# Optimization experiments

Measured on AMD Instinct MI355X. Metric: run time of the kernel, lower is better.

## Reference

```python
import jax, jax.numpy as jnp
import numpy as np

V, E, H, OUT, L = 32000, 512, 512, 2, 2
S, B = 512, 64


def setup_inputs() -> dict:
    key = jax.random.key(0)
    ks = jax.random.split(key, 8)
    sc_w = float(np.sqrt(6.0 / (H + (E + H))))  # xavier_uniform bound-ish scale
    inp = {
        "texts": jax.random.randint(ks[0], (S, B), 0, V, dtype=jnp.int64),
        "emb": jax.random.normal(ks[1], (V, E), jnp.float32) * 0.05,
        "Wf": jax.random.normal(ks[2], (L, H, E + H), jnp.float32) * sc_w,
        "bf": jnp.zeros((L, H, 1), jnp.float32),
        "Wi": jax.random.normal(ks[3], (L, H, E + H), jnp.float32) * sc_w,
        "bi": jnp.zeros((L, H, 1), jnp.float32),
        "Wo": jax.random.normal(ks[4], (L, H, E + H), jnp.float32) * sc_w,
        "bo": jnp.zeros((L, H, 1), jnp.float32),
        "Wc": jax.random.normal(ks[5], (L, H, E + H), jnp.float32) * sc_w,
        "bc": jnp.zeros((L, H, 1), jnp.float32),
        "Wy": jax.random.normal(ks[6], (OUT, H), jnp.float32) * 0.05,
        "by": jnp.zeros((OUT, 1), jnp.float32),
    }
    return inp


def reference(texts, emb, Wf, bf, Wi, bi, Wo, bo, Wc, bc, Wy, by):
    seq_len, batch = texts.shape
    num_layers, hidden = Wf.shape[0], Wf.shape[1]
    # embedded: [S, E, B] (matches torch permute(1,2,0) of [B,S,E])
    x_seq = jnp.transpose(emb[texts], (0, 2, 1))

    h0 = jnp.zeros((hidden, batch), x_seq.dtype)
    c0 = jnp.zeros((hidden, batch), x_seq.dtype)

    def step(carry, x):
        h, c = carry  # NOTE: single (h, c) shared across layers, as in source
        for l in range(num_layers):
            cat = jnp.concatenate([h, x], axis=0)  # [H+E, B]
            ft = jax.nn.sigmoid(Wf[l] @ cat + bf[l])
            it = jax.nn.sigmoid(Wi[l] @ cat + bi[l])
            chat = jnp.tanh(Wc[l] @ cat + bc[l])
            c = ft * c + it * chat
            ot = jax.nn.sigmoid(Wo[l] @ cat + bo[l])
            h = ot * jnp.tanh(c)
            x = h
        return (h, c), None

    (h, _), _ = jax.lax.scan(step, (h0, c0), x_seq)
    y = h.T @ Wy.T + by.T  # [B, OUT]
    return jnp.squeeze(y, axis=1) if y.shape[1] == 1 else y
```

## Files before the change

kernel.cpp:

```cpp
#include <hip/hip_runtime.h>


typedef _Float16 f16;
typedef _Float16 f16x8 __attribute__((ext_vector_type(8)));
typedef float f32x4 __attribute__((ext_vector_type(4)));
typedef unsigned int u32;
typedef unsigned long long u64;
typedef unsigned short u16;

constexpr int Hn = 512, En = 512, Bn = 64, Sn = 512, OUTn = 2;
constexpr int NG = 4, GB = 32, BS = 16, RPB = 16;
constexpr int NB = NG * GB;
constexpr int NT = 512;
constexpr int RING = 16;
constexpr u32 SENT = 0xFFFFFFFFu;

constexpr size_t XB_OFF = 0;
constexpr size_t XB_SZ  = (size_t)NG * Sn * 16 * 64 * 16;
constexpr size_t RG_OFF = XB_OFF + XB_SZ;
constexpr size_t RG_SZ  = (size_t)NG * RING * 16384;

__device__ __forceinline__ float sig_(float x) { return 1.f / (1.f + expf(-x)); }

__device__ __forceinline__ void astore(u32* p, u32 v) {
  __hip_atomic_store(p, v, __ATOMIC_RELAXED, __HIP_MEMORY_SCOPE_AGENT);
}
__device__ __forceinline__ u64 aload64(const u64* p) {
  return __hip_atomic_load(p, __ATOMIC_RELAXED, __HIP_MEMORY_SCOPE_AGENT);
}
__device__ __forceinline__ bool okw(u64 x) {
  return ((u32)x != SENT) && ((u32)(x >> 32) != SENT);
}
__device__ __forceinline__ void poll2(const u64* p0, const u64* p1, f16x8& a, f16x8& b) {
  union U { f16x8 v; u64 q[2]; } ua, ub;
  int guard = 0;
  for (;;) {
    ua.q[0] = aload64(p0); ua.q[1] = aload64(p0 + 1);
    ub.q[0] = aload64(p1); ub.q[1] = aload64(p1 + 1);
    if (okw(ua.q[0]) && okw(ua.q[1]) && okw(ub.q[0]) && okw(ub.q[1])) break;
    if (++guard > (1 << 21)) break;
  }
  a = ua.v; b = ub.v;
}

union uf16 { f16 f; u16 u; };

__device__ __forceinline__ int fl_idx(int k, int col) {
  return (((k >> 5) * 64 + (((k >> 3) & 3) * 16) + col) << 3) + (k & 7);
}

__global__ void __launch_bounds__(256) xb_fill(
    const int* __restrict__ texts, const float* __restrict__ emb,
    f16x8* __restrict__ xb)
{
  const int bidx = blockIdx.x;
  const int g = bidx >> 9, t = bidx & (Sn - 1);
  const int tid = threadIdx.x;
  f16x8* dst = xb + (size_t)bidx * 1024;
  for (int slot = tid; slot < 1024; slot += 256) {
    int s = slot >> 6, sl = slot & 63, kg = sl >> 4, b = sl & 15;
    int idx = texts[t * Bn + g * BS + b];
    const float* er = emb + (size_t)idx * En + s * 32 + kg * 8;
    f16x8 v;
    #pragma unroll
    for (int j = 0; j < 8; ++j) v[j] = (f16)er[j];
    dst[slot] = v;
  }
}

__global__ void __launch_bounds__(NT) lstm_mfma(
    const float* __restrict__ Wf, const float* __restrict__ bf,
    const float* __restrict__ Wi, const float* __restrict__ bi,
    const float* __restrict__ Wo, const float* __restrict__ bo,
    const float* __restrict__ Wc, const float* __restrict__ bc,
    const float* __restrict__ Wy, const float* __restrict__ by,
    float* __restrict__ out, const f16x8* __restrict__ xb,
    u32* __restrict__ ringBase)
{
  __shared__ f16x8 sWAh[4][16][64];
  __shared__ f16x8 sXB[16][64];
  __shared__ f16x8 sHB[1024];
  __shared__ float sAccP[2][64][17];
  __shared__ float sAccX[64][17];
  __shared__ float sBiasX[64], sBias1[64];
  __shared__ float sC[16][16];
  __shared__ float sRed[16][2][4];

  const int tid = threadIdx.x;
  const int bid = blockIdx.x;
  const int g = bid & 3;
  const int rank = bid >> 2;
  const int w = tid >> 6, l = tid & 63;
  const int mt = w & 3, kh = w >> 2;
  const int col = l & 15, rb = (l >> 4) << 2;

  const float* Wg[4] = {Wf, Wi, Wc, Wo};
  const float* Bg[4] = {bf, bi, bc, bo};

  u32* ringG = ringBase + (size_t)g * RING * 4096;
  const f16x8* xbG = xb + (size_t)g * Sn * 1024;

  for (int i = 0; i < 8; ++i) {
    int slot = tid * 8 + i;
    int sl = slot & 63, s = (slot >> 6) & 15, m4 = slot >> 10;
    const float* row = Wg[m4] + (size_t)(rank * RPB + (sl & 15)) * (En + Hn);
    int k0 = s * 32 + (sl >> 4) * 8;
    f16x8 v;
    #pragma unroll
    for (int j = 0; j < 8; ++j) v[j] = (f16)row[k0 + j];
    sWAh[m4][s][sl] = v;
  }
  f16x8 afr1[8];
  {
    const float* row = Wg[mt] + (size_t)(Hn + rank * RPB + (l & 15)) * (En + Hn);
    #pragma unroll
    for (int i = 0; i < 8; ++i) {
      int k0 = (kh * 8 + i) * 32 + (l >> 4) * 8;
      f16x8 v;
      #pragma unroll
      for (int j = 0; j < 8; ++j) v[j] = (f16)(row[k0 + j] + row[k0 + j + Hn]);
      afr1[i] = v;
    }
  }
  f16x8 axf[16];
  if (kh == 1) {
    const float* row = Wg[mt] + (size_t)(rank * RPB + (l & 15)) * (En + Hn);
    #pragma unroll
    for (int i = 0; i < 16; ++i) {
      int k0 = Hn + i * 32 + (l >> 4) * 8;
      f16x8 v;
      #pragma unroll
      for (int j = 0; j < 8; ++j) v[j] = (f16)row[k0 + j];
      axf[i] = v;
    }
  }
  if (tid < 64) {
    int gate = tid >> 4, hr = tid & 15;
    sBiasX[tid] = Bg[gate][rank * RPB + hr];
    sBias1[tid] = Bg[gate][Hn + rank * RPB + hr];
  }
  if (tid < 256) sC[tid >> 4][tid & 15] = 0.f;
  if (w >= 4) {
    #pragma unroll
    for (int j = 0; j < 4; ++j) sXB[(w - 4) * 4 + j][l] = xbG[((w - 4) * 4 + j) * 64 + l];
  }
  __syncthreads();
  if (kh == 1) {
    f32x4 acc = {0.f, 0.f, 0.f, 0.f};
    #pragma unroll
    for (int s = 0; s < 16; ++s)
      acc = __builtin_amdgcn_mfma_f32_16x16x32_f16(axf[s], sXB[s][l], acc, 0, 0, 0);
    #pragma unroll
    for (int v = 0; v < 4; ++v) sAccX[mt * 16 + rb + v][col] = acc[v];
  }

  for (int t = 0; t < Sn; ++t) {
    const int qA = 2 * t;
    u32* bufRA = ringG + (size_t)(qA & 15) * 4096;
    u32* bufWA = ringG + (size_t)((qA + 1) & 15) * 4096;
    u32* bufCA = ringG + (size_t)((qA + 9) & 15) * 4096;

    if (tid >= 128 && tid < 256) astore(bufCA + rank * 128 + (tid - 128), SENT);
    f16x8 xp[4];
    if (w >= 4) {
      const int tn = (t + 1 < Sn) ? t + 1 : t;
      const f16x8* xbt = xbG + (size_t)tn * 1024;
      #pragma unroll
      for (int j = 0; j < 4; ++j) xp[j] = xbt[((w - 4) * 4 + j) * 64 + l];
    }
    {
      const u64* src = (const u64*)bufRA;
      f16x8 a, b;
      poll2(src + (w * 128 + l) * 2, src + (w * 128 + 64 + l) * 2, a, b);
      sHB[w * 128 + l] = a; sHB[w * 128 + 64 + l] = b;
    }
    if (w >= 4) {
      #pragma unroll
      for (int j = 0; j < 4; ++j) sXB[(w - 4) * 4 + j][l] = xp[j];
    }
    __syncthreads();
    {
      f32x4 acc = {0.f, 0.f, 0.f, 0.f};
      #pragma unroll
      for (int i = 0; i < 8; ++i) {
        int s = kh * 8 + i;
        acc = __builtin_amdgcn_mfma_f32_16x16x32_f16(sWAh[mt][s][l], sHB[s * 64 + l], acc, 0, 0, 0);
      }
      #pragma unroll
      for (int v = 0; v < 4; ++v) sAccP[kh][mt * 16 + rb + v][col] = acc[v];
    }
    __syncthreads();
    if (tid < 128) {
      int q8 = tid >> 4, b = tid & 15;
      u32 pk = 0;
      #pragma unroll
      for (int j = 0; j < 2; ++j) {
        int hr = 2 * q8 + j;
        float af = sAccP[0][ 0 + hr][b] + sAccP[1][ 0 + hr][b] + sAccX[ 0 + hr][b] + sBiasX[ 0 + hr];
        float ai = sAccP[0][16 + hr][b] + sAccP[1][16 + hr][b] + sAccX[16 + hr][b] + sBiasX[16 + hr];
        float ac = sAccP[0][32 + hr][b] + sAccP[1][32 + hr][b] + sAccX[32 + hr][b] + sBiasX[32 + hr];
        float ao = sAccP[0][48 + hr][b] + sAccP[1][48 + hr][b] + sAccX[48 + hr][b] + sBiasX[48 + hr];
        float ft = sig_(af), it = sig_(ai), ch = tanhf(ac), ot = sig_(ao);
        float c = ft * sC[hr][b] + it * ch;
        sC[hr][b] = c;
        uf16 hv; hv.f = (f16)(ot * tanhf(c));
        pk |= (u32)hv.u << (16 * j);
      }
      int k0 = rank * RPB + 2 * q8;
      int slot = (k0 >> 5) * 64 + ((k0 >> 3) & 3) * 16 + b;
      astore(bufWA + slot * 4 + (q8 & 3), pk);
    }

    u32* bufWB = ringG + (size_t)((qA + 2) & 15) * 4096;
    u32* bufCB = ringG + (size_t)((qA + 10) & 15) * 4096;
    if (tid >= 128 && tid < 256) astore(bufCB + rank * 128 + (tid - 128), SENT);
    {
      const u64* src = (const u64*)bufWA;
      f16x8 a, b;
      poll2(src + (w * 128 + l) * 2, src + (w * 128 + 64 + l) * 2, a, b);
      sHB[w * 128 + l] = a; sHB[w * 128 + 64 + l] = b;
    }
    __syncthreads();
    {
      f32x4 acc = {0.f, 0.f, 0.f, 0.f};
      #pragma unroll
      for (int i = 0; i < 8; ++i)
        acc = __builtin_amdgcn_mfma_f32_16x16x32_f16(afr1[i], sHB[(kh * 8 + i) * 64 + l], acc, 0, 0, 0);
      #pragma unroll
      for (int v = 0; v < 4; ++v) sAccP[kh][mt * 16 + rb + v][col] = acc[v];
    }
    __syncthreads();
    if (tid < 128) {
      int q8 = tid >> 4, b = tid & 15;
      u32 pk = 0;
      #pragma unroll
      for (int j = 0; j < 2; ++j) {
        int hr = 2 * q8 + j;
        float af = sAccP[0][ 0 + hr][b] + sAccP[1][ 0 + hr][b] + sBias1[ 0 + hr];
        float ai = sAccP[0][16 + hr][b] + sAccP[1][16 + hr][b] + sBias1[16 + hr];
        float ac = sAccP[0][32 + hr][b] + sAccP[1][32 + hr][b] + sBias1[32 + hr];
        float ao = sAccP[0][48 + hr][b] + sAccP[1][48 + hr][b] + sBias1[48 + hr];
        float ft = sig_(af), it = sig_(ai), ch = tanhf(ac), ot = sig_(ao);
        float c = ft * sC[hr][b] + it * ch;
        sC[hr][b] = c;
        uf16 hv; hv.f = (f16)(ot * tanhf(c));
        pk |= (u32)hv.u << (16 * j);
      }
      int k0 = rank * RPB + 2 * q8;
      int slot = (k0 >> 5) * 64 + ((k0 >> 3) & 3) * 16 + b;
      astore(bufWB + slot * 4 + (q8 & 3), pk);
    }
    if (kh == 1 && t + 1 < Sn) {
      f32x4 acc = {0.f, 0.f, 0.f, 0.f};
      #pragma unroll
      for (int s = 0; s < 16; ++s)
        acc = __builtin_amdgcn_mfma_f32_16x16x32_f16(axf[s], sXB[s][l], acc, 0, 0, 0);
      #pragma unroll
      for (int v = 0; v < 4; ++v) sAccX[mt * 16 + rb + v][col] = acc[v];
    }
  }

  if (rank == 0) {
    const u64* fin = (const u64*)(ringG + (size_t)((2 * Sn) & 15) * 4096);
    u64* dst = (u64*)sHB;
    for (int i = tid; i < 2048; i += NT) {
      u64 v = aload64(fin + i);
      int guard = 0;
      while (!okw(v)) { v = aload64(fin + i); if (++guard > (1 << 21)) break; }
      dst[i] = v;
    }
    __syncthreads();
    const f16* tmp = (const f16*)sHB;
    if (tid < 128) {
      int b = tid >> 3, o = (tid >> 2) & 1, kc = tid & 3;
      float p = 0.f;
      for (int kk = 0; kk < 128; ++kk) {
        int k = kc * 128 + kk;
        p += (float)tmp[fl_idx(k, b)] * Wy[o * Hn + k];
      }
      sRed[b][o][kc] = p;
    }
    __syncthreads();
    if (tid < 32) {
      int b2 = tid >> 1, o2 = tid & 1;
      float s = by[o2];
      #pragma unroll
      for (int q = 0; q < 4; ++q) s += sRed[b2][o2][q];
      out[(g * BS + b2) * OUTn + o2] = s;
    }
  }
}

extern "C" void kernel_launch(void* const* d_in, const int* in_sizes, int n_in,
                              void* d_out, int out_size, void* d_ws, size_t ws_size,
                              hipStream_t stream) {
  const int*   texts = (const int*)d_in[0];
  const float* emb   = (const float*)d_in[1];
  const float* Wf    = (const float*)d_in[2];
  const float* bf    = (const float*)d_in[3];
  const float* Wi    = (const float*)d_in[4];
  const float* bi    = (const float*)d_in[5];
  const float* Wo    = (const float*)d_in[6];
  const float* bo    = (const float*)d_in[7];
  const float* Wc    = (const float*)d_in[8];
  const float* bc    = (const float*)d_in[9];
  const float* Wy    = (const float*)d_in[10];
  const float* by    = (const float*)d_in[11];
  float* out = (float*)d_out;

  f16x8* xbuf    = (f16x8*)((char*)d_ws + XB_OFF);
  u32*   ringBase = (u32*)((char*)d_ws + RG_OFF);

  hipMemsetAsync((void*)ringBase, 0xFF, RG_SZ, stream);
  for (int g = 0; g < NG; ++g)
    hipMemsetAsync((void*)((char*)ringBase + (size_t)g * RING * 16384), 0x00, 16384, stream);

  xb_fill<<<dim3(NG * Sn), dim3(256), 0, stream>>>(texts, emb, xbuf);

  void* args[] = {(void*)&Wf, (void*)&bf, (void*)&Wi, (void*)&bi,
                  (void*)&Wo, (void*)&bo, (void*)&Wc, (void*)&bc, (void*)&Wy, (void*)&by,
                  (void*)&out, (void*)&xbuf, (void*)&ringBase};
  hipLaunchCooperativeKernel((const void*)lstm_mfma, dim3(NB), dim3(NT), args, 0, stream);
}
```

Baseline: 2.669 ms.

## Pack two batch groups per block with per-half LDS flag sync

Halves the grid from 128 to 64 blocks, so each block serves two batch groups, with each 4-wave half handling one group. Block-wide __syncthreads inside the time loop are replaced by LDS flag spinning between the waves of a half. Global ring polling now uses one 16-byte load with the sc1 cache bit per fragment. The input projection is computed directly from global memory by all waves after each step, and each wave does two MFMA gate tiles. The aim is fewer blocks taking part in the cross-block handoff and less barrier stall, at the cost of more work per block and fragile hand-rolled intra-block synchronisation.

Result: slower. 4.717 ms (+76.7%).

```diff
diff --git a/kernel.cpp b/kernel.cpp
--- a/kernel.cpp
+++ b/kernel.cpp
@@ -9,9 +9,8 @@
 typedef unsigned short u16;
 
 constexpr int Hn = 512, En = 512, Bn = 64, Sn = 512, OUTn = 2;
-constexpr int NG = 4, GB = 32, BS = 16, RPB = 16;
-constexpr int NB = NG * GB;
-constexpr int NT = 512;
+constexpr int NG = 4, BS = 16, RPB = 16;
+constexpr int NB = 64, NT = 512;
 constexpr int RING = 16;
 constexpr u32 SENT = 0xFFFFFFFFu;
 
@@ -31,16 +30,34 @@
 __device__ __forceinline__ bool okw(u64 x) {
   return ((u32)x != SENT) && ((u32)(x >> 32) != SENT);
 }
-__device__ __forceinline__ void poll2(const u64* p0, const u64* p1, f16x8& a, f16x8& b) {
-  union U { f16x8 v; u64 q[2]; } ua, ub;
+
+__device__ __forceinline__ f16x8 poll16(const u32* p) {
+  union { f16x8 v; u32 d[4]; } u;
   int guard = 0;
-  for (;;) {
-    ua.q[0] = aload64(p0); ua.q[1] = aload64(p0 + 1);
-    ub.q[0] = aload64(p1); ub.q[1] = aload64(p1 + 1);
-    if (okw(ua.q[0]) && okw(ua.q[1]) && okw(ub.q[0]) && okw(ub.q[1])) break;
-    if (++guard > (1 << 21)) break;
-  }
-  a = ua.v; b = ub.v;
+  do {
+    asm volatile("global_load_dwordx4 %0, %1, off sc1\n\ts_waitcnt vmcnt(0)"
+                 : "=&v"(u.v) : "v"(p) : "memory");
+    if ((u.d[0] != SENT) & (u.d[1] != SENT) & (u.d[2] != SENT) & (u.d[3] != SENT)) break;
+  } while (++guard < (1 << 17));
+  return u.v;
+}
+
+__device__ __forceinline__ void spin_ge(volatile u32* f, u32 q) {
+  int guard = 0;
+  while (*f < q) { if (++guard > (1 << 17)) break; }
+  __builtin_amdgcn_sched_barrier(0);
+}
+__device__ __forceinline__ void spin4(volatile u32* f, u32 q) {
+  int guard = 0;
+  while (f[0] < q || f[1] < q || f[2] < q || f[3] < q) {
+    if (++guard > (1 << 17)) break;
+  }
+  __builtin_amdgcn_sched_barrier(0);
+}
+__device__ __forceinline__ void set_flag(volatile u32* f, u32 q, int lane) {
+  asm volatile("s_waitcnt lgkmcnt(0)" ::: "memory");
+  __builtin_amdgcn_sched_barrier(0);
+  if (lane == 0) *f = q;
 }
 
 union uf16 { f16 f; u16 u; };
@@ -78,20 +95,25 @@
     u32* __restrict__ ringBase)
 {
   __shared__ f16x8 sWAh[4][16][64];
-  __shared__ f16x8 sXB[16][64];
-  __shared__ f16x8 sHB[1024];
-  __shared__ float sAccP[2][64][17];
-  __shared__ float sAccX[64][17];
+  __shared__ f16x8 sHB[2][1024];
+  __shared__ float sAccP[2][2][64][17];
+  __shared__ float sAccX[2][64][17];
   __shared__ float sBiasX[64], sBias1[64];
-  __shared__ float sC[16][16];
-  __shared__ float sRed[16][2][4];
+  __shared__ float sC[2][16][16];
+  __shared__ float sRed[2][16][2][4];
+  __shared__ volatile u32 sStg[2][4];
+  __shared__ volatile u32 sAcF[2][4];
+  __shared__ volatile u32 sGtF[2][2];
 
   const int tid = threadIdx.x;
   const int bid = blockIdx.x;
-  const int g = bid & 3;
-  const int rank = bid >> 2;
+  const int rank = bid >> 1;
+  const int jj = bid & 1;
   const int w = tid >> 6, l = tid & 63;
-  const int mt = w & 3, kh = w >> 2;
+  const int s = w >> 2;
+  const int u = w & 3;
+  const int p = u & 1, kh = u >> 1;
+  const int g = jj * 2 + s;
   const int col = l & 15, rb = (l >> 4) << 2;
 
   const float* Wg[4] = {Wf, Wi, Wc, Wo};
@@ -102,29 +124,30 @@
 
   for (int i = 0; i < 8; ++i) {
     int slot = tid * 8 + i;
-    int sl = slot & 63, s = (slot >> 6) & 15, m4 = slot >> 10;
+    int sl = slot & 63, ss = (slot >> 6) & 15, m4 = slot >> 10;
     const float* row = Wg[m4] + (size_t)(rank * RPB + (sl & 15)) * (En + Hn);
-    int k0 = s * 32 + (sl >> 4) * 8;
+    int k0 = ss * 32 + (sl >> 4) * 8;
     f16x8 v;
     #pragma unroll
     for (int j = 0; j < 8; ++j) v[j] = (f16)row[k0 + j];
-    sWAh[m4][s][sl] = v;
-  }
-  f16x8 afr1[8];
-  {
-    const float* row = Wg[mt] + (size_t)(Hn + rank * RPB + (l & 15)) * (En + Hn);
+    sWAh[m4][ss][sl] = v;
+  }
+  f16x8 afr1[2][8];
+  #pragma unroll
+  for (int mi = 0; mi < 2; ++mi) {
+    const float* row = Wg[2 * p + mi] + (size_t)(Hn + rank * RPB + (l & 15)) * (En + Hn);
     #pragma unroll
     for (int i = 0; i < 8; ++i) {
       int k0 = (kh * 8 + i) * 32 + (l >> 4) * 8;
       f16x8 v;
       #pragma unroll
       for (int j = 0; j < 8; ++j) v[j] = (f16)(row[k0 + j] + row[k0 + j + Hn]);
-      afr1[i] = v;
+      afr1[mi][i] = v;
     }
   }
   f16x8 axf[16];
-  if (kh == 1) {
-    const float* row = Wg[mt] + (size_t)(rank * RPB + (l & 15)) * (En + Hn);
+  {
+    const float* row = Wg[u] + (size_t)(rank * RPB + (l & 15)) * (En + Hn);
     #pragma unroll
     for (int i = 0; i < 16; ++i) {
       int k0 = Hn + i * 32 + (l >> 4) * 8;
@@ -139,155 +162,182 @@
     sBiasX[tid] = Bg[gate][rank * RPB + hr];
     sBias1[tid] = Bg[gate][Hn + rank * RPB + hr];
   }
-  if (tid < 256) sC[tid >> 4][tid & 15] = 0.f;
-  if (w >= 4) {
-    #pragma unroll
-    for (int j = 0; j < 4; ++j) sXB[(w - 4) * 4 + j][l] = xbG[((w - 4) * 4 + j) * 64 + l];
-  }
+  if (tid < 512) sC[tid >> 8][(tid >> 4) & 15][tid & 15] = 0.f;
+  if (tid < 4) { sStg[0][tid] = 0; sStg[1][tid] = 0; sAcF[0][tid] = 0; sAcF[1][tid] = 0; }
+  if (tid < 2) { sGtF[0][tid] = 0; sGtF[1][tid] = 0; }
   __syncthreads();
-  if (kh == 1) {
-    f32x4 acc = {0.f, 0.f, 0.f, 0.f};
-    #pragma unroll
-    for (int s = 0; s < 16; ++s)
-      acc = __builtin_amdgcn_mfma_f32_16x16x32_f16(axf[s], sXB[s][l], acc, 0, 0, 0);
-    #pragma unroll
-    for (int v = 0; v < 4; ++v) sAccX[mt * 16 + rb + v][col] = acc[v];
-  }
+
+  {
+    f32x4 ax = {0.f, 0.f, 0.f, 0.f};
+    #pragma unroll
+    for (int ks = 0; ks < 16; ++ks)
+      ax = __builtin_amdgcn_mfma_f32_16x16x32_f16(axf[ks], xbG[ks * 64 + l], ax, 0, 0, 0);
+    #pragma unroll
+    for (int v = 0; v < 4; ++v) sAccX[s][u * 16 + rb + v][col] = ax[v];
+  }
+
+  const int fbase = kh * 512 + p * 256;
 
   for (int t = 0; t < Sn; ++t) {
-    const int qA = 2 * t;
-    u32* bufRA = ringG + (size_t)(qA & 15) * 4096;
-    u32* bufWA = ringG + (size_t)((qA + 1) & 15) * 4096;
-    u32* bufCA = ringG + (size_t)((qA + 9) & 15) * 4096;
-
-    if (tid >= 128 && tid < 256) astore(bufCA + rank * 128 + (tid - 128), SENT);
-    f16x8 xp[4];
-    if (w >= 4) {
-      const int tn = (t + 1 < Sn) ? t + 1 : t;
-      const f16x8* xbt = xbG + (size_t)tn * 1024;
-      #pragma unroll
-      for (int j = 0; j < 4; ++j) xp[j] = xbt[((w - 4) * 4 + j) * 64 + l];
-    }
+    u32* rdA = ringG + (size_t)((2 * t) & 15) * 4096;
+    u32* wrA = ringG + (size_t)((2 * t + 1) & 15) * 4096;
+    u32* clA = ringG + (size_t)((2 * t + 9) & 15) * 4096;
+
     {
-      const u64* src = (const u64*)bufRA;
-      f16x8 a, b;
-      poll2(src + (w * 128 + l) * 2, src + (w * 128 + 64 + l) * 2, a, b);
-      sHB[w * 128 + l] = a; sHB[w * 128 + 64 + l] = b;
-    }
-    if (w >= 4) {
-      #pragma unroll
-      for (int j = 0; j < 4; ++j) sXB[(w - 4) * 4 + j][l] = xp[j];
-    }
-    __syncthreads();
+      const u32 q = 2 * t + 1;
+      f16x8 fr0 = poll16(rdA + (fbase + 0 * 64 + l) * 4);
+      f16x8 fr1 = poll16(rdA + (fbase + 1 * 64 + l) * 4);
+      f16x8 fr2 = poll16(rdA + (fbase + 2 * 64 + l) * 4);
+      f16x8 fr3 = poll16(rdA + (fbase + 3 * 64 + l) * 4);
+      spin4(&sAcF[s][0], q - 1);
+      sHB[s][fbase + 0 * 64 + l] = fr0;
+      sHB[s][fbase + 1 * 64 + l] = fr1;
+      sHB[s][fbase + 2 * 64 + l] = fr2;
+      sHB[s][fbase + 3 * 64 + l] = fr3;
+      set_flag(&sStg[s][u], q, l);
+      spin_ge(&sStg[s][u ^ 1], q);
+      spin_ge(&sGtF[s][0], q - 1);
+      spin_ge(&sGtF[s][1], q - 1);
+      f32x4 a0 = {0.f, 0.f, 0.f, 0.f}, a1 = {0.f, 0.f, 0.f, 0.f};
+      #pragma unroll
+      for (int i = 0; i < 8; ++i) {
+        int ks = kh * 8 + i;
+        f16x8 bf = sHB[s][ks * 64 + l];
+        a0 = __builtin_amdgcn_mfma_f32_16x16x32_f16(sWAh[2 * p + 0][ks][l], bf, a0, 0, 0, 0);
+        a1 = __builtin_amdgcn_mfma_f32_16x16x32_f16(sWAh[2 * p + 1][ks][l], bf, a1, 0, 0, 0);
+      }
+      #pragma unroll
+      for (int v = 0; v < 4; ++v) {
+        sAccP[s][kh][(2 * p + 0) * 16 + rb + v][col] = a0[v];
+        sAccP[s][kh][(2 * p + 1) * 16 + rb + v][col] = a1[v];
+      }
+      set_flag(&sAcF[s][u], q, l);
+      if (u < 2) {
+        spin4(&sAcF[s][0], q);
+        int gt = u * 64 + l, q8 = gt >> 4, b = gt & 15;
+        u32 pk = 0;
+        #pragma unroll
+        for (int j = 0; j < 2; ++j) {
+          int hr = 2 * q8 + j;
+          float af = sAccP[s][0][ 0 + hr][b] + sAccP[s][1][ 0 + hr][b] + sAccX[s][ 0 + hr][b] + sBiasX[ 0 + hr];
+          float ai = sAccP[s][0][16 + hr][b] + sAccP[s][1][16 + hr][b] + sAccX[s][16 + hr][b] + sBiasX[16 + hr];
+          float ac = sAccP[s][0][32 + hr][b] + sAccP[s][1][32 + hr][b] + sAccX[s][32 + hr][b] + sBiasX[32 + hr];
+          float ao = sAccP[s][0][48 + hr][b] + sAccP[s][1][48 + hr][b] + sAccX[s][48 + hr][b] + sBiasX[48 + hr];
+          float ft = sig_(af), it = sig_(ai), ch = tanhf(ac), ot = sig_(ao);
+          float c = ft * sC[s][hr][b] + it * ch;
+          sC[s][hr][b] = c;
+          uf16 hv; hv.f = (f16)(ot * tanhf(c));
+          pk |= (u32)hv.u << (16 * j);
+        }
+        int k0 = rank * RPB + 2 * q8;
+        int slot = (k0 >> 5) * 64 + ((k0 >> 3) & 3) * 16 + b;
+        astore(wrA + slot * 4 + (q8 & 3), pk);
+        __builtin_amdgcn_sched_barrier(0);
+        if (l == 0) sGtF[s][u] = q;
+      } else {
+        astore(clA + rank * 128 + (u - 2) * 64 + l, SENT);
+      }
+    }
+
     {
-      f32x4 acc = {0.f, 0.f, 0.f, 0.f};
+      const u32 q = 2 * t + 2;
+      u32* rdB = wrA;
+      u32* wrB = ringG + (size_t)((2 * t + 2) & 15) * 4096;
+      u32* clB = ringG + (size_t)((2 * t + 10) & 15) * 4096;
+      f16x8 fr0 = poll16(rdB + (fbase + 0 * 64 + l) * 4);
+      f16x8 fr1 = poll16(rdB + (fbase + 1 * 64 + l) * 4);
+      f16x8 fr2 = poll16(rdB + (fbase + 2 * 64 + l) * 4);
+      f16x8 fr3 = poll16(rdB + (fbase + 3 * 64 + l) * 4);
+      spin4(&sAcF[s][0], q - 1);
+      sHB[s][fbase + 0 * 64 + l] = fr0;
+      sHB[s][fbase + 1 * 64 + l] = fr1;
+      sHB[s][fbase + 2 * 64 + l] = fr2;
+      sHB[s][fbase + 3 * 64 + l] = fr3;
+      set_flag(&sStg[s][u], q, l);
+      spin_ge(&sStg[s][u ^ 1], q);
+      spin_ge(&sGtF[s][0], q - 1);
+      spin_ge(&sGtF[s][1], q - 1);
+      f32x4 a0 = {0.f, 0.f, 0.f, 0.f}, a1 = {0.f, 0.f, 0.f, 0.f};
       #pragma unroll
       for (int i = 0; i < 8; ++i) {
-        int s = kh * 8 + i;
-        acc = __builtin_amdgcn_mfma_f32_16x16x32_f16(sWAh[mt][s][l], sHB[s * 64 + l], acc, 0, 0, 0);
-      }
-      #pragma unroll
-      for (int v = 0; v < 4; ++v) sAccP[kh][mt * 16 + rb + v][col] = acc[v];
-    }
-    __syncthreads();
-    if (tid < 128) {
-      int q8 = tid >> 4, b = tid & 15;
-      u32 pk = 0;
-      #pragma unroll
-      for (int j = 0; j < 2; ++j) {
-        int hr = 2 * q8 + j;
-        float af = sAccP[0][ 0 + hr][b] + sAccP[1][ 0 + hr][b] + sAccX[ 0 + hr][b] + sBiasX[ 0 + hr];
-        float ai = sAccP[0][16 + hr][b] + sAccP[1][16 + hr][b] + sAccX[16 + hr][b] + sBiasX[16 + hr];
-        float ac = sAccP[0][32 + hr][b] + sAccP[1][32 + hr][b] + sAccX[32 + hr][b] + sBiasX[32 + hr];
-        float ao = sAccP[0][48 + hr][b] + sAccP[1][48 + hr][b] + sAccX[48 + hr][b] + sBiasX[48 + hr];
-        float ft = sig_(af), it = sig_(ai), ch = tanhf(ac), ot = sig_(ao);
-        float c = ft * sC[hr][b] + it * ch;
-        sC[hr][b] = c;
-        uf16 hv; hv.f = (f16)(ot * tanhf(c));
-        pk |= (u32)hv.u << (16 * j);
-      }
-      int k0 = rank * RPB + 2 * q8;
-      int slot = (k0 >> 5) * 64 + ((k0 >> 3) & 3) * 16 + b;
-      astore(bufWA + slot * 4 + (q8 & 3), pk);
-    }
-
-    u32* bufWB = ringG + (size_t)((qA + 2) & 15) * 4096;
-    u32* bufCB = ringG + (size_t)((qA + 10) & 15) * 4096;
-    if (tid >= 128 && tid < 256) astore(bufCB + rank * 128 + (tid - 128), SENT);
-    {
-      const u64* src = (const u64*)bufWA;
-      f16x8 a, b;
-      poll2(src + (w * 128 + l) * 2, src + (w * 128 + 64 + l) * 2, a, b);
-      sHB[w * 128 + l] = a; sHB[w * 128 + 64 + l] = b;
-    }
-    __syncthreads();
-    {
-      f32x4 acc = {0.f, 0.f, 0.f, 0.f};
-      #pragma unroll
-      for (int i = 0; i < 8; ++i)
-        acc = __builtin_amdgcn_mfma_f32_16x16x32_f16(afr1[i], sHB[(kh * 8 + i) * 64 + l], acc, 0, 0, 0);
-      #pragma unroll
-      for (int v = 0; v < 4; ++v) sAccP[kh][mt * 16 + rb + v][col] = acc[v];
-    }
-    __syncthreads();
-    if (tid < 128) {
-      int q8 = tid >> 4, b = tid & 15;
-      u32 pk = 0;
-      #pragma unroll
-      for (int j = 0; j < 2; ++j) {
-        int hr = 2 * q8 + j;
-        float af = sAccP[0][ 0 + hr][b] + sAccP[1][ 0 + hr][b] + sBias1[ 0 + hr];
-        float ai = sAccP[0][16 + hr][b] + sAccP[1][16 + hr][b] + sBias1[16 + hr];
-        float ac = sAccP[0][32 + hr][b] + sAccP[1][32 + hr][b] + sBias1[32 + hr];
-        float ao = sAccP[0][48 + hr][b] + sAccP[1][48 + hr][b] + sBias1[48 + hr];
-        float ft = sig_(af), it = sig_(ai), ch = tanhf(ac), ot = sig_(ao);
-        float c = ft * sC[hr][b] + it * ch;
-        sC[hr][b] = c;
-        uf16 hv; hv.f = (f16)(ot * tanhf(c));
-        pk |= (u32)hv.u << (16 * j);
-      }
-      int k0 = rank * RPB + 2 * q8;
-      int slot = (k0 >> 5) * 64 + ((k0 >> 3) & 3) * 16 + b;
-      astore(bufWB + slot * 4 + (q8 & 3), pk);
-    }
-    if (kh == 1 && t + 1 < Sn) {
-      f32x4 acc = {0.f, 0.f, 0.f, 0.f};
-      #pragma unroll
-      for (int s = 0; s < 16; ++s)
-        acc = __builtin_amdgcn_mfma_f32_16x16x32_f16(axf[s], sXB[s][l], acc, 0, 0, 0);
-      #pragma unroll
-      for (int v = 0; v < 4; ++v) sAccX[mt * 16 + rb + v][col] = acc[v];
-    }
-  }
-
+        int ks = kh * 8 + i;
+        f16x8 bf = sHB[s][ks * 64 + l];
+        a0 = __builtin_amdgcn_mfma_f32_16x16x32_f16(afr1[0][i], bf, a0, 0, 0, 0);
+        a1 = __builtin_amdgcn_mfma_f32_16x16x32_f16(afr1[1][i], bf, a1, 0, 0, 0);
+      }
+      #pragma unroll
+      for (int v = 0; v < 4; ++v) {
+        sAccP[s][kh][(2 * p + 0) * 16 + rb + v][col] = a0[v];
+        sAccP[s][kh][(2 * p + 1) * 16 + rb + v][col] = a1[v];
+      }
+      set_flag(&sAcF[s][u], q, l);
+      if (u < 2) {
+        spin4(&sAcF[s][0], q);
+        int gt = u * 64 + l, q8 = gt >> 4, b = gt & 15;
+        u32 pk = 0;
+        #pragma unroll
+        for (int j = 0; j < 2; ++j) {
+          int hr = 2 * q8 + j;
+          float af = sAccP[s][0][ 0 + hr][b] + sAccP[s][1][ 0 + hr][b] + sBias1[ 0 + hr];
+          float ai = sAccP[s][0][16 + hr][b] + sAccP[s][1][16 + hr][b] + sBias1[16 + hr];
+          float ac = sAccP[s][0][32 + hr][b] + sAccP[s][1][32 + hr][b] + sBias1[32 + hr];
+          float ao = sAccP[s][0][48 + hr][b] + sAccP[s][1][48 + hr][b] + sBias1[48 + hr];
+          float ft = sig_(af), it = sig_(ai), ch = tanhf(ac), ot = sig_(ao);
+          float c = ft * sC[s][hr][b] + it * ch;
+          sC[s][hr][b] = c;
+          uf16 hv; hv.f = (f16)(ot * tanhf(c));
+          pk |= (u32)hv.u << (16 * j);
+        }
+        int k0 = rank * RPB + 2 * q8;
+        int slot = (k0 >> 5) * 64 + ((k0 >> 3) & 3) * 16 + b;
+        astore(wrB + slot * 4 + (q8 & 3), pk);
+        __builtin_amdgcn_sched_barrier(0);
+        if (l == 0) sGtF[s][u] = q;
+      } else {
+        astore(clB + rank * 128 + (u - 2) * 64 + l, SENT);
+      }
+      if (t + 1 < Sn) {
+        const f16x8* xbt = xbG + (size_t)(t + 1) * 1024;
+        f32x4 ax = {0.f, 0.f, 0.f, 0.f};
+        #pragma unroll
+        for (int ks = 0; ks < 16; ++ks)
+          ax = __builtin_amdgcn_mfma_f32_16x16x32_f16(axf[ks], xbt[ks * 64 + l], ax, 0, 0, 0);
+        #pragma unroll
+        for (int v = 0; v < 4; ++v) sAccX[s][u * 16 + rb + v][col] = ax[v];
+      }
+    }
+  }
+
+  __syncthreads();
+  const int qq = (w & 3) * 64 + l;
   if (rank == 0) {
-    const u64* fin = (const u64*)(ringG + (size_t)((2 * Sn) & 15) * 4096);
-    u64* dst = (u64*)sHB;
-    for (int i = tid; i < 2048; i += NT) {
+    const u64* fin = (const u64*)ringG;
+    u64* dst = (u64*)&sHB[s][0];
+    for (int i = qq; i < 2048; i += 256) {
       u64 v = aload64(fin + i);
       int guard = 0;
-      while (!okw(v)) { v = aload64(fin + i); if (++guard > (1 << 21)) break; }
+      while (!okw(v)) { v = aload64(fin + i); if (++guard > (1 << 17)) break; }
       dst[i] = v;
     }
-    __syncthreads();
-    const f16* tmp = (const f16*)sHB;
-    if (tid < 128) {
-      int b = tid >> 3, o = (tid >> 2) & 1, kc = tid & 3;
-      float p = 0.f;
-      for (int kk = 0; kk < 128; ++kk) {
-        int k = kc * 128 + kk;
-        p += (float)tmp[fl_idx(k, b)] * Wy[o * Hn + k];
-      }
-      sRed[b][o][kc] = p;
-    }
-    __syncthreads();
-    if (tid < 32) {
-      int b2 = tid >> 1, o2 = tid & 1;
-      float s = by[o2];
-      #pragma unroll
-      for (int q = 0; q < 4; ++q) s += sRed[b2][o2][q];
-      out[(g * BS + b2) * OUTn + o2] = s;
-    }
+  }
+  __syncthreads();
+  if (rank == 0 && qq < 128) {
+    const f16* tmp = (const f16*)&sHB[s][0];
+    int b = qq >> 3, o = (qq >> 2) & 1, kc = qq & 3;
+    float pv = 0.f;
+    for (int kk = 0; kk < 128; ++kk) {
+      int k = kc * 128 + kk;
+      pv += (float)tmp[fl_idx(k, b)] * Wy[o * Hn + k];
+    }
+    sRed[s][b][o][kc] = pv;
+  }
+  __syncthreads();
+  if (rank == 0 && qq < 32) {
+    int b2 = qq >> 1, o2 = qq & 1;
+    float sm = by[o2];
+    #pragma unroll
+    for (int r2 = 0; r2 < 4; ++r2) sm += sRed[s][b2][o2][r2];
+    out[(g * BS + b2) * OUTn + o2] = sm;
   }
 }
 
@@ -308,7 +358,7 @@
   const float* by    = (const float*)d_in[11];
   float* out = (float*)d_out;
 
-  f16x8* xbuf    = (f16x8*)((char*)d_ws + XB_OFF);
+  f16x8* xbuf     = (f16x8*)((char*)d_ws + XB_OFF);
   u32*   ringBase = (u32*)((char*)d_ws + RG_OFF);
 
   hipMemsetAsync((void*)ringBase, 0xFF, RG_SZ, stream);
```

## Split recurrent matmul by K across 8 waves and poll ring directly into registers

Applied to the files above, without the earlier changes.

Each of the 8 waves now polls two 16-byte chunks of h from the global ring straight into registers, using inline global_load_dwordx4 with sc1, and feeds them directly to MFMAs for all four gates. The shared h staging buffer and one __syncthreads per half-step are removed. Each wave now handles a K slice for all gates instead of one gate and half of K. The elementwise step therefore has to reduce 8 partial sums per gate, and sAccP grows to eight slices. The x-projection reads x tiles directly from global memory instead of staging them in shared memory, and the poll timeout guard is shortened.

After: 2.515 ms. -5.8%, faster.

```diff
diff --git a/kernel.cpp b/kernel.cpp
--- a/kernel.cpp
+++ b/kernel.cpp
@@ -31,15 +31,18 @@
 __device__ __forceinline__ bool okw(u64 x) {
   return ((u32)x != SENT) && ((u32)(x >> 32) != SENT);
 }
-__device__ __forceinline__ void poll2(const u64* p0, const u64* p1, f16x8& a, f16x8& b) {
-  union U { f16x8 v; u64 q[2]; } ua, ub;
+
+__device__ __forceinline__ void poll2x(const u32* p0, const u32* p1, f16x8& a, f16x8& b) {
+  union { f16x8 v; u32 d[4]; } ua, ub;
   int guard = 0;
-  for (;;) {
-    ua.q[0] = aload64(p0); ua.q[1] = aload64(p0 + 1);
-    ub.q[0] = aload64(p1); ub.q[1] = aload64(p1 + 1);
-    if (okw(ua.q[0]) && okw(ua.q[1]) && okw(ub.q[0]) && okw(ub.q[1])) break;
-    if (++guard > (1 << 21)) break;
-  }
+  do {
+    asm volatile("global_load_dwordx4 %0, %2, off sc1\n\t"
+                 "global_load_dwordx4 %1, %3, off sc1\n\t"
+                 "s_waitcnt vmcnt(0)"
+                 : "=&v"(ua.v), "=&v"(ub.v) : "v"(p0), "v"(p1) : "memory");
+    if ((ua.d[0] != SENT) & (ua.d[1] != SENT) & (ua.d[2] != SENT) & (ua.d[3] != SENT) &
+        (ub.d[0] != SENT) & (ub.d[1] != SENT) & (ub.d[2] != SENT) & (ub.d[3] != SENT)) break;
+  } while (++guard < (1 << 17));
   a = ua.v; b = ub.v;
 }
 
@@ -78,9 +81,7 @@
     u32* __restrict__ ringBase)
 {
   __shared__ f16x8 sWAh[4][16][64];
-  __shared__ f16x8 sXB[16][64];
-  __shared__ f16x8 sHB[1024];
-  __shared__ float sAccP[2][64][17];
+  __shared__ float sAccP[8][64][17];
   __shared__ float sAccX[64][17];
   __shared__ float sBiasX[64], sBias1[64];
   __shared__ float sC[16][16];
@@ -91,7 +92,6 @@
   const int g = bid & 3;
   const int rank = bid >> 2;
   const int w = tid >> 6, l = tid & 63;
-  const int mt = w & 3, kh = w >> 2;
   const int col = l & 15, rb = (l >> 4) << 2;
 
   const float* Wg[4] = {Wf, Wi, Wc, Wo};
@@ -102,29 +102,30 @@
 
   for (int i = 0; i < 8; ++i) {
     int slot = tid * 8 + i;
-    int sl = slot & 63, s = (slot >> 6) & 15, m4 = slot >> 10;
+    int sl = slot & 63, ss = (slot >> 6) & 15, m4 = slot >> 10;
     const float* row = Wg[m4] + (size_t)(rank * RPB + (sl & 15)) * (En + Hn);
-    int k0 = s * 32 + (sl >> 4) * 8;
+    int k0 = ss * 32 + (sl >> 4) * 8;
     f16x8 v;
     #pragma unroll
     for (int j = 0; j < 8; ++j) v[j] = (f16)row[k0 + j];
-    sWAh[m4][s][sl] = v;
-  }
-  f16x8 afr1[8];
-  {
-    const float* row = Wg[mt] + (size_t)(Hn + rank * RPB + (l & 15)) * (En + Hn);
-    #pragma unroll
-    for (int i = 0; i < 8; ++i) {
-      int k0 = (kh * 8 + i) * 32 + (l >> 4) * 8;
+    sWAh[m4][ss][sl] = v;
+  }
+  f16x8 afr1[4][2];
+  #pragma unroll
+  for (int m = 0; m < 4; ++m) {
+    const float* row = Wg[m] + (size_t)(Hn + rank * RPB + (l & 15)) * (En + Hn);
+    #pragma unroll
+    for (int i = 0; i < 2; ++i) {
+      int k0 = (2 * w + i) * 32 + (l >> 4) * 8;
       f16x8 v;
       #pragma unroll
       for (int j = 0; j < 8; ++j) v[j] = (f16)(row[k0 + j] + row[k0 + j + Hn]);
-      afr1[i] = v;
+      afr1[m][i] = v;
     }
   }
   f16x8 axf[16];
-  if (kh == 1) {
-    const float* row = Wg[mt] + (size_t)(rank * RPB + (l & 15)) * (En + Hn);
+  if (w >= 4) {
+    const float* row = Wg[w - 4] + (size_t)(rank * RPB + (l & 15)) * (En + Hn);
     #pragma unroll
     for (int i = 0; i < 16; ++i) {
       int k0 = Hn + i * 32 + (l >> 4) * 8;
@@ -140,54 +141,42 @@
     sBias1[tid] = Bg[gate][Hn + rank * RPB + hr];
   }
   if (tid < 256) sC[tid >> 4][tid & 15] = 0.f;
+  __syncthreads();
+
   if (w >= 4) {
-    #pragma unroll
-    for (int j = 0; j < 4; ++j) sXB[(w - 4) * 4 + j][l] = xbG[((w - 4) * 4 + j) * 64 + l];
-  }
-  __syncthreads();
-  if (kh == 1) {
-    f32x4 acc = {0.f, 0.f, 0.f, 0.f};
+    f32x4 ax = {0.f, 0.f, 0.f, 0.f};
     #pragma unroll
     for (int s = 0; s < 16; ++s)
-      acc = __builtin_amdgcn_mfma_f32_16x16x32_f16(axf[s], sXB[s][l], acc, 0, 0, 0);
-    #pragma unroll
-    for (int v = 0; v < 4; ++v) sAccX[mt * 16 + rb + v][col] = acc[v];
+      ax = __builtin_amdgcn_mfma_f32_16x16x32_f16(axf[s], xbG[s * 64 + l], ax, 0, 0, 0);
+    #pragma unroll
+    for (int v = 0; v < 4; ++v) sAccX[(w - 4) * 16 + rb + v][col] = ax[v];
   }
 
   for (int t = 0; t < Sn; ++t) {
-    const int qA = 2 * t;
-    u32* bufRA = ringG + (size_t)(qA & 15) * 4096;
-    u32* bufWA = ringG + (size_t)((qA + 1) & 15) * 4096;
-    u32* bufCA = ringG + (size_t)((qA + 9) & 15) * 4096;
-
-    if (tid >= 128 && tid < 256) astore(bufCA + rank * 128 + (tid - 128), SENT);
-    f16x8 xp[4];
-    if (w >= 4) {
-      const int tn = (t + 1 < Sn) ? t + 1 : t;
-      const f16x8* xbt = xbG + (size_t)tn * 1024;
-      #pragma unroll
-      for (int j = 0; j < 4; ++j) xp[j] = xbt[((w - 4) * 4 + j) * 64 + l];
-    }
+    u32* rdA = ringG + (size_t)((2 * t) & 15) * 4096;
+    u32* wrA = ringG + (size_t)((2 * t + 1) & 15) * 4096;
+    u32* clA = ringG + (size_t)((2 * t + 9) & 15) * 4096;
+
+    if (tid >= 128 && tid < 256) astore(clA + rank * 128 + (tid - 128), SENT);
     {
-      const u64* src = (const u64*)bufRA;
-      f16x8 a, b;
-      poll2(src + (w * 128 + l) * 2, src + (w * 128 + 64 + l) * 2, a, b);
-      sHB[w * 128 + l] = a; sHB[w * 128 + 64 + l] = b;
-    }
-    if (w >= 4) {
-      #pragma unroll
-      for (int j = 0; j < 4; ++j) sXB[(w - 4) * 4 + j][l] = xp[j];
-    }
-    __syncthreads();
-    {
-      f32x4 acc = {0.f, 0.f, 0.f, 0.f};
-      #pragma unroll
-      for (int i = 0; i < 8; ++i) {
-        int s = kh * 8 + i;
-        acc = __builtin_amdgcn_mfma_f32_16x16x32_f16(sWAh[mt][s][l], sHB[s * 64 + l], acc, 0, 0, 0);
+      f16x8 b0, b1;
+      poll2x(rdA + (2 * w * 64 + l) * 4, rdA + ((2 * w + 1) * 64 + l) * 4, b0, b1);
+      f32x4 a0 = {0.f, 0.f, 0.f, 0.f}, a1 = a0, a2 = a0, a3 = a0;
+      a0 = __builtin_amdgcn_mfma_f32_16x16x32_f16(sWAh[0][2 * w][l], b0, a0, 0, 0, 0);
+      a1 = __builtin_amdgcn_mfma_f32_16x16x32_f16(sWAh[1][2 * w][l], b0, a1, 0, 0, 0);
+      a2 = __builtin_amdgcn_mfma_f32_16x16x32_f16(sWAh[2][2 * w][l], b0, a2, 0, 0, 0);
+      a3 = __builtin_amdgcn_mfma_f32_16x16x32_f16(sWAh[3][2 * w][l], b0, a3, 0, 0, 0);
+      a0 = __builtin_amdgcn_mfma_f32_16x16x32_f16(sWAh[0][2 * w + 1][l], b1, a0, 0, 0, 0);
+      a1 = __builtin_amdgcn_mfma_f32_16x16x32_f16(sWAh[1][2 * w + 1][l], b1, a1, 0, 0, 0);
+      a2 = __builtin_amdgcn_mfma_f32_16x16x32_f16(sWAh[2][2 * w + 1][l], b1, a2, 0, 0, 0);
+      a3 = __builtin_amdgcn_mfma_f32_16x16x32_f16(sWAh[3][2 * w + 1][l], b1, a3, 0, 0, 0);
+      #pragma unroll
+      for (int v = 0; v < 4; ++v) {
+        sAccP[w][ 0 + rb + v][col] = a0[v];
+        sAccP[w][16 + rb + v][col] = a1[v];
+        sAccP[w][32 + rb + v][col] = a2[v];
+        sAccP[w][48 + rb + v][col] = a3[v];
       }
-      #pragma unroll
-      for (int v = 0; v < 4; ++v) sAccP[kh][mt * 16 + rb + v][col] = acc[v];
     }
     __syncthreads();
     if (tid < 128) {
@@ -196,10 +185,17 @@
       #pragma unroll
       for (int j = 0; j < 2; ++j) {
         int hr = 2 * q8 + j;
-        float af = sAccP[0][ 0 + hr][b] + sAccP[1][ 0 + hr][b] + sAccX[ 0 + hr][b] + sBiasX[ 0 + hr];
-        float ai = sAccP[0][16 + hr][b] + sAccP[1][16 + hr][b] + sAccX[16 + hr][b] + sBiasX[16 + hr];
-        float ac = sAccP[0][32 + hr][b] + sAccP[1][32 + hr][b] + sAccX[32 + hr][b] + sBiasX[32 + hr];
-        float ao = sAccP[0][48 + hr][b] + sAccP[1][48 + hr][b] + sAccX[48 + hr][b] + sBiasX[48 + hr];
+        float af = sAccX[ 0 + hr][b] + sBiasX[ 0 + hr];
+        float ai = sAccX[16 + hr][b] + sBiasX[16 + hr];
+        float ac = sAccX[32 + hr][b] + sBiasX[32 + hr];
+        float ao = sAccX[48 + hr][b] + sBiasX[48 + hr];
+        #pragma unroll
+        for (int ww = 0; ww < 8; ++ww) {
+          af += sAccP[ww][ 0 + hr][b];
+          ai += sAccP[ww][16 + hr][b];
+          ac += sAccP[ww][32 + hr][b];
+          ao += sAccP[ww][48 + hr][b];
+        }
         float ft = sig_(af), it = sig_(ai), ch = tanhf(ac), ot = sig_(ao);
         float c = ft * sC[hr][b] + it * ch;
         sC[hr][b] = c;
@@ -208,26 +204,31 @@
       }
       int k0 = rank * RPB + 2 * q8;
       int slot = (k0 >> 5) * 64 + ((k0 >> 3) & 3) * 16 + b;
-      astore(bufWA + slot * 4 + (q8 & 3), pk);
-    }
-
-    u32* bufWB = ringG + (size_t)((qA + 2) & 15) * 4096;
-    u32* bufCB = ringG + (size_t)((qA + 10) & 15) * 4096;
-    if (tid >= 128 && tid < 256) astore(bufCB + rank * 128 + (tid - 128), SENT);
+      astore(wrA + slot * 4 + (q8 & 3), pk);
+    }
+
+    u32* wrB = ringG + (size_t)((2 * t + 2) & 15) * 4096;
+    u32* clB = ringG + (size_t)((2 * t + 10) & 15) * 4096;
+    if (tid >= 128 && tid < 256) astore(clB + rank * 128 + (tid - 128), SENT);
     {
-      const u64* src = (const u64*)bufWA;
-      f16x8 a, b;
-      poll2(src + (w * 128 + l) * 2, src + (w * 128 + 64 + l) * 2, a, b);
-      sHB[w * 128 + l] = a; sHB[w * 128 + 64 + l] = b;
-    }
-    __syncthreads();
-    {
-      f32x4 acc = {0.f, 0.f, 0.f, 0.f};
-      #pragma unroll
-      for (int i = 0; i < 8; ++i)
-        acc = __builtin_amdgcn_mfma_f32_16x16x32_f16(afr1[i], sHB[(kh * 8 + i) * 64 + l], acc, 0, 0, 0);
-      #pragma unroll
-      for (int v = 0; v < 4; ++v) sAccP[kh][mt * 16 + rb + v][col] = acc[v];
+      f16x8 b0, b1;
+      poll2x(wrA + (2 * w * 64 + l) * 4, wrA + ((2 * w + 1) * 64 + l) * 4, b0, b1);
+      f32x4 a0 = {0.f, 0.f, 0.f, 0.f}, a1 = a0, a2 = a0, a3 = a0;
+      a0 = __builtin_amdgcn_mfma_f32_16x16x32_f16(afr1[0][0], b0, a0, 0, 0, 0);
+      a1 = __builtin_amdgcn_mfma_f32_16x16x32_f16(afr1[1][0], b0, a1, 0, 0, 0);
+      a2 = __builtin_amdgcn_mfma_f32_16x16x32_f16(afr1[2][0], b0, a2, 0, 0, 0);
+      a3 = __builtin_amdgcn_mfma_f32_16x16x32_f16(afr1[3][0], b0, a3, 0, 0, 0);
+      a0 = __builtin_amdgcn_mfma_f32_16x16x32_f16(afr1[0][1], b1, a0, 0, 0, 0);
+      a1 = __builtin_amdgcn_mfma_f32_16x16x32_f16(afr1[1][1], b1, a1, 0, 0, 0);
+      a2 = __builtin_amdgcn_mfma_f32_16x16x32_f16(afr1[2][1], b1, a2, 0, 0, 0);
+      a3 = __builtin_amdgcn_mfma_f32_16x16x32_f16(afr1[3][1], b1, a3, 0, 0, 0);
+      #pragma unroll
+      for (int v = 0; v < 4; ++v) {
+        sAccP[w][ 0 + rb + v][col] = a0[v];
+        sAccP[w][16 + rb + v][col] = a1[v];
+        sAccP[w][32 + rb + v][col] = a2[v];
+        sAccP[w][48 + rb + v][col] = a3[v];
+      }
     }
     __syncthreads();
     if (tid < 128) {
@@ -236,10 +237,17 @@
       #pragma unroll
       for (int j = 0; j < 2; ++j) {
         int hr = 2 * q8 + j;
-        float af = sAccP[0][ 0 + hr][b] + sAccP[1][ 0 + hr][b] + sBias1[ 0 + hr];
-        float ai = sAccP[0][16 + hr][b] + sAccP[1][16 + hr][b] + sBias1[16 + hr];
-        float ac = sAccP[0][32 + hr][b] + sAccP[1][32 + hr][b] + sBias1[32 + hr];
-        float ao = sAccP[0][48 + hr][b] + sAccP[1][48 + hr][b] + sBias1[48 + hr];
+        float af = sBias1[ 0 + hr];
+        float ai = sBias1[16 + hr];
+        float ac = sBias1[32 + hr];
+        float ao = sBias1[48 + hr];
+        #pragma unroll
+        for (int ww = 0; ww < 8; ++ww) {
+          af += sAccP[ww][ 0 + hr][b];
+          ai += sAccP[ww][16 + hr][b];
+          ac += sAccP[ww][32 + hr][b];
+          ao += sAccP[ww][48 + hr][b];
+        }
         float ft = sig_(af), it = sig_(ai), ch = tanhf(ac), ot = sig_(ao);
         float c = ft * sC[hr][b] + it * ch;
         sC[hr][b] = c;
@@ -248,46 +256,48 @@
       }
       int k0 = rank * RPB + 2 * q8;
       int slot = (k0 >> 5) * 64 + ((k0 >> 3) & 3) * 16 + b;
-      astore(bufWB + slot * 4 + (q8 & 3), pk);
-    }
-    if (kh == 1 && t + 1 < Sn) {
-      f32x4 acc = {0.f, 0.f, 0.f, 0.f};
+      astore(wrB + slot * 4 + (q8 & 3), pk);
+    }
+    if (w >= 4 && t + 1 < Sn) {
+      const f16x8* xbt = xbG + (size_t)(t + 1) * 1024;
+      f32x4 ax = {0.f, 0.f, 0.f, 0.f};
       #pragma unroll
       for (int s = 0; s < 16; ++s)
-        acc = __builtin_amdgcn_mfma_f32_16x16x32_f16(axf[s], sXB[s][l], acc, 0, 0, 0);
-      #pragma unroll
-      for (int v = 0; v < 4; ++v) sAccX[mt * 16 + rb + v][col] = acc[v];
-    }
-  }
-
+        ax = __builtin_amdgcn_mfma_f32_16x16x32_f16(axf[s], xbt[s * 64 + l], ax, 0, 0, 0);
+      #pragma unroll
+      for (int v = 0; v < 4; ++v) sAccX[(w - 4) * 16 + rb + v][col] = ax[v];
+    }
+  }
+
+  __syncthreads();
   if (rank == 0) {
-    const u64* fin = (const u64*)(ringG + (size_t)((2 * Sn) & 15) * 4096);
-    u64* dst = (u64*)sHB;
+    const u64* fin = (const u64*)ringG;
+    u64* dst = (u64*)&sWAh[0][0][0];
     for (int i = tid; i < 2048; i += NT) {
       u64 v = aload64(fin + i);
       int guard = 0;
-      while (!okw(v)) { v = aload64(fin + i); if (++guard > (1 << 21)) break; }
+      while (!okw(v)) { v = aload64(fin + i); if (++guard > (1 << 17)) break; }
       dst[i] = v;
     }
-    __syncthreads();
-    const f16* tmp = (const f16*)sHB;
-    if (tid < 128) {
-      int b = tid >> 3, o = (tid >> 2) & 1, kc = tid & 3;
-      float p = 0.f;
-      for (int kk = 0; kk < 128; ++kk) {
-        int k = kc * 128 + kk;
-        p += (float)tmp[fl_idx(k, b)] * Wy[o * Hn + k];
-      }
-      sRed[b][o][kc] = p;
-    }
-    __syncthreads();
-    if (tid < 32) {
-      int b2 = tid >> 1, o2 = tid & 1;
-      float s = by[o2];
-      #pragma unroll
-      for (int q = 0; q < 4; ++q) s += sRed[b2][o2][q];
-      out[(g * BS + b2) * OUTn + o2] = s;
-    }
+  }
+  __syncthreads();
+  if (rank == 0 && tid < 128) {
+    const f16* tmp = (const f16*)&sWAh[0][0][0];
+    int b = tid >> 3, o = (tid >> 2) & 1, kc = tid & 3;
+    float p = 0.f;
+    for (int kk = 0; kk < 128; ++kk) {
+      int k = kc * 128 + kk;
+      p += (float)tmp[fl_idx(k, b)] * Wy[o * Hn + k];
+    }
+    sRed[b][o][kc] = p;
+  }
+  __syncthreads();
+  if (rank == 0 && tid < 32) {
+    int b2 = tid >> 1, o2 = tid & 1;
+    float s = by[o2];
+    #pragma unroll
+    for (int q = 0; q < 4; ++q) s += sRed[b2][o2][q];
+    out[(g * BS + b2) * OUTn + o2] = s;
   }
 }
 
@@ -308,7 +318,7 @@
   const float* by    = (const float*)d_in[11];
   float* out = (float*)d_out;
 
-  f16x8* xbuf    = (f16x8*)((char*)d_ws + XB_OFF);
+  f16x8* xbuf     = (f16x8*)((char*)d_ws + XB_OFF);
   u32*   ringBase = (u32*)((char*)d_ws + RG_OFF);
 
   hipMemsetAsync((void*)ringBase, 0xFF, RG_SZ, stream);
```
